# Optimization experiments

Measured on AMD Instinct MI355X. Metric: run time of the kernel, lower is better.

Reference implementation:

```python
import jax, jax.numpy as jnp
import numpy as np

MARGIN = 0.3

def _pairwise_euclid(x):
    # torch.cdist(x, x, p=2): [N, N] Euclidean distances, zero-safe sqrt
    sq_norms = jnp.sum(x * x, axis=1)                       # [N]
    sq = sq_norms[:, None] + sq_norms[None, :] - 2.0 * (x @ x.T)
    sq = jnp.maximum(sq, 0.0)
    safe = jnp.where(sq > 0.0, sq, 1.0)
    return jnp.where(sq > 0.0, jnp.sqrt(safe), 0.0)

def setup_inputs() -> dict:
    key = jax.random.key(0)
    k1, k2 = jax.random.split(key)
    features = jax.random.normal(k1, (4096, 512), dtype=jnp.float32)
    labels = jax.random.randint(k2, (4096,), 0, 256, dtype=jnp.int64)
    return {"features": features, "labels": labels}

def reference(features, labels):
    n = features.shape[0]
    dist = _pairwise_euclid(features)                       # [N, N]
    pos_mask = labels[:, None] == labels[None, :]           # includes self
    neg_inf = jnp.float32(-np.inf)
    pos_inf = jnp.float32(np.inf)
    hardest_pos = jnp.max(jnp.where(pos_mask, dist, neg_inf), axis=1)   # [N]
    hardest_neg = jnp.min(jnp.where(pos_mask, pos_inf, dist), axis=1)   # [N]
    valid = jnp.sum(pos_mask, axis=1) > 1                   # >1 positives incl. self
    per_row = jax.nn.relu(hardest_pos - hardest_neg + MARGIN)
    loss = jnp.sum(jnp.where(valid, per_row, 0.0)) / n
    return loss
```

## Files before the change

### kernel.cpp

```cpp
#include <hip/hip_runtime.h>

#define NROWS 4096
#define DIM   512
#define MARGIN 0.3f

typedef _Float16 f16;
typedef _Float16 f16x8 __attribute__((ext_vector_type(8)));
typedef float    f32x4 __attribute__((ext_vector_type(4)));

__global__ void prep_kernel(const float* __restrict__ X,
                            float* __restrict__ norms, f16* __restrict__ Xh,
                            unsigned* __restrict__ hp, unsigned* __restrict__ hn) {
    int t = threadIdx.x;
    int wave = t >> 6, lane = t & 63;
    int row  = blockIdx.x * 4 + wave;
    const float4* p = (const float4*)(X + (size_t)row * DIM + lane * 8);
    float4 a = p[0], b = p[1];
    float s = a.x*a.x + a.y*a.y + a.z*a.z + a.w*a.w
            + b.x*b.x + b.y*b.y + b.z*b.z + b.w*b.w;
    #pragma unroll
    for (int o = 32; o; o >>= 1) s += __shfl_xor(s, o);
    if (lane == 0) norms[row] = s;

    f16x8 h;
    h[0] = (f16)a.x; h[1] = (f16)a.y; h[2] = (f16)a.z; h[3] = (f16)a.w;
    h[4] = (f16)b.x; h[5] = (f16)b.y; h[6] = (f16)b.z; h[7] = (f16)b.w;
    int K0 = lane >> 2, c = lane & 3;
    int R = row >> 7, rw = row & 127, rg = rw >> 4, r = rw & 15;
    size_t unit = (size_t)(R * 16 + K0) * 512 + rg * 64 + c * 16 + r;
    *(f16x8*)(Xh + unit * 8) = h;

    int g = blockIdx.x * 256 + t;
    if (g < NROWS) { hp[g] = 0u; hn[g] = 0x7f800000u; }
}

__device__ inline void gload_lds16(const f16* g, f16* l) {
    __builtin_amdgcn_global_load_lds(
        (const __attribute__((address_space(1))) void*)g,
        (__attribute__((address_space(3))) void*)l, 16, 0, 0);
}

__device__ inline void stage_tile(const f16* __restrict__ At, const f16* __restrict__ Bt,
                                  f16* buf, int qb, int lane) {
    const f16* base = (qb < 512) ? (At + (size_t)qb * 8) : (Bt + (size_t)(qb - 512) * 8);
    #pragma unroll
    for (int c2 = 0; c2 < 4; ++c2)
        gload_lds16(base + (size_t)(c2 * 64 + lane) * 8, buf + (size_t)(qb + c2 * 64) * 8);
}

__global__ __launch_bounds__(256, 3) void mfma_dist_kernel(
        const f16* __restrict__ Xh, const int* __restrict__ labels,
        const float* __restrict__ norms,
        unsigned* __restrict__ hp, unsigned* __restrict__ hn) {
    __shared__ __align__(16) f16 S[3 * 8192];

    const int t    = threadIdx.x;
    const int lane = t & 63, w = t >> 6;
    const int l15  = lane & 15, l4 = lane >> 4;

    int bthw = blockIdx.x;
    int bt = (bthw & 7) * 66 + (bthw >> 3);

    int bx = (int)((sqrtf(8.0f * bt + 1.0f) - 1.0f) * 0.5f);
    while ((bx + 1) * (bx + 2) / 2 <= bt) ++bx;
    while (bx * (bx + 1) / 2 > bt) --bx;
    int by = bt - bx * (bx + 1) / 2;

    const int wr = w >> 1, wc = w & 1;
    const int qb = w * 256;

    const f16* Abase = Xh + (size_t)(by * 16) * 4096;
    const f16* Bbase = Xh + (size_t)(bx * 16) * 4096;

    f32x4 zero = {0.f, 0.f, 0.f, 0.f};
    f32x4 acc[4][4];
    #pragma unroll
    for (int m = 0; m < 4; ++m)
        #pragma unroll
        for (int n = 0; n < 4; ++n) acc[m][n] = zero;

    stage_tile(Abase,        Bbase,        S,        qb, lane);
    stage_tile(Abase + 4096, Bbase + 4096, S + 8192, qb, lane);
    __builtin_amdgcn_sched_barrier(0);

    #pragma unroll
    for (int kt = 0; kt < 16; ++kt) {
        f16* cur = S + (kt % 3) * 8192;
        if (kt == 15) asm volatile("s_waitcnt vmcnt(0)" ::: "memory");
        else          asm volatile("s_waitcnt vmcnt(4)" ::: "memory");
        __builtin_amdgcn_sched_barrier(0);
        __builtin_amdgcn_s_barrier();
        __builtin_amdgcn_sched_barrier(0);

        if (kt + 2 < 16)
            stage_tile(Abase + (size_t)(kt + 2) * 4096,
                       Bbase + (size_t)(kt + 2) * 4096,
                       S + ((kt + 2) % 3) * 8192, qb, lane);
        __builtin_amdgcn_sched_barrier(0);

        f16x8 af[4], bf[4];
        #pragma unroll
        for (int m = 0; m < 4; ++m)
            af[m] = *(const f16x8*)&cur[(size_t)((wr * 4 + m) * 64 + l4 * 16 + l15) * 8];
        #pragma unroll
        for (int n = 0; n < 4; ++n)
            bf[n] = *(const f16x8*)&cur[(size_t)(512 + (wc * 4 + n) * 64 + l4 * 16 + l15) * 8];
        #pragma unroll
        for (int m = 0; m < 4; ++m)
            #pragma unroll
            for (int n = 0; n < 4; ++n)
                acc[m][n] = __builtin_amdgcn_mfma_f32_16x16x32_f16(af[m], bf[n], acc[m][n], 0, 0, 0);
        __builtin_amdgcn_sched_barrier(0);
    }

    const int wrow = by * 128 + wr * 64;
    const int wcol = bx * 128 + wc * 64;
    const float FINF = __uint_as_float(0x7f800000u);

    int lj[4]; float nj[4];
    #pragma unroll
    for (int n = 0; n < 4; ++n) {
        int gc = wcol + n * 16 + l15; lj[n] = labels[gc]; nj[n] = norms[gc];
    }
    int li[16]; float ni[16];
    #pragma unroll
    for (int m = 0; m < 4; ++m)
        #pragma unroll
        for (int r = 0; r < 4; ++r) {
            int gr = wrow + m * 16 + l4 * 4 + r;
            li[m * 4 + r] = labels[gr]; ni[m * 4 + r] = norms[gr];
        }

    float cp[4], cn[4];
    #pragma unroll
    for (int n = 0; n < 4; ++n) { cp[n] = 0.f; cn[n] = FINF; }

    #pragma unroll
    for (int m = 0; m < 4; ++m) {
        #pragma unroll
        for (int r = 0; r < 4; ++r) {
            float rp = 0.f, rn = FINF;
            #pragma unroll
            for (int n = 0; n < 4; ++n) {
                float sq = fmaxf(fmaf(-2.f, acc[m][n][r], ni[m * 4 + r] + nj[n]), 0.f);
                bool same = (li[m * 4 + r] == lj[n]);
                rp = same ? fmaxf(rp, sq) : rp;
                rn = same ? rn : fminf(rn, sq);
                cp[n] = same ? fmaxf(cp[n], sq) : cp[n];
                cn[n] = same ? cn[n] : fminf(cn[n], sq);
            }
            #pragma unroll
            for (int o = 8; o; o >>= 1) {
                rp = fmaxf(rp, __shfl_xor(rp, o));
                rn = fminf(rn, __shfl_xor(rn, o));
            }
            if (l15 == 0) {
                int gr = wrow + m * 16 + l4 * 4 + r;
                atomicMax(&hp[gr], __float_as_uint(rp));
                atomicMin(&hn[gr], __float_as_uint(rn));
            }
        }
    }
    #pragma unroll
    for (int n = 0; n < 4; ++n) {
        float p = cp[n], q = cn[n];
        p = fmaxf(p, __shfl_xor(p, 16)); q = fminf(q, __shfl_xor(q, 16));
        p = fmaxf(p, __shfl_xor(p, 32)); q = fminf(q, __shfl_xor(q, 32));
        if (l4 == 0) {
            int gc = wcol + n * 16 + l15;
            atomicMax(&hp[gc], __float_as_uint(p));
            atomicMin(&hn[gc], __float_as_uint(q));
        }
    }
}

__global__ void norms_init_kernel(const float* __restrict__ X,
                                  float* __restrict__ norms,
                                  unsigned* __restrict__ hp, unsigned* __restrict__ hn) {
    int wave = threadIdx.x >> 6;
    int lane = threadIdx.x & 63;
    int row  = blockIdx.x * 4 + wave;
    const float4* xr = (const float4*)(X + (size_t)row * DIM);
    float4 a = xr[lane];
    float4 b = xr[lane + 64];
    float s = a.x*a.x + a.y*a.y + a.z*a.z + a.w*a.w
            + b.x*b.x + b.y*b.y + b.z*b.z + b.w*b.w;
    #pragma unroll
    for (int o = 32; o; o >>= 1) s += __shfl_xor(s, o);
    if (lane == 0) norms[row] = s;
    int g = blockIdx.x * 256 + threadIdx.x;
    if (g < NROWS) { hp[g] = 0u; hn[g] = 0x7f800000u; }
}

#define BK  32
#define PAD 68
__global__ __launch_bounds__(256) void dist_fp32_kernel(
        const float* __restrict__ X, const int* __restrict__ labels,
        const float* __restrict__ norms,
        unsigned* __restrict__ hp, unsigned* __restrict__ hn) {
    __shared__ __align__(16) float As[BK][PAD];
    __shared__ __align__(16) float Bs[BK][PAD];
    const int t  = threadIdx.x;
    const int tx = t & 15, ty = t >> 4;
    const int row0 = blockIdx.y * 64, col0 = blockIdx.x * 64;

    float acc[4][4] = {};
    for (int k0 = 0; k0 < DIM; k0 += BK) {
        #pragma unroll
        for (int l = 0; l < 2; ++l) {
            int idx = t + l * 256;
            int r = idx >> 3, fc = idx & 7;
            float4 va = *(const float4*)(X + (size_t)(row0 + r) * DIM + k0 + fc * 4);
            float4 vb = *(const float4*)(X + (size_t)(col0 + r) * DIM + k0 + fc * 4);
            As[fc*4+0][r] = va.x; As[fc*4+1][r] = va.y;
            As[fc*4+2][r] = va.z; As[fc*4+3][r] = va.w;
            Bs[fc*4+0][r] = vb.x; Bs[fc*4+1][r] = vb.y;
            Bs[fc*4+2][r] = vb.z; Bs[fc*4+3][r] = vb.w;
        }
        __syncthreads();
        #pragma unroll
        for (int kk = 0; kk < BK; ++kk) {
            float4 a = *(const float4*)&As[kk][ty * 4];
            float4 b = *(const float4*)&Bs[kk][tx * 4];
            float av[4] = {a.x, a.y, a.z, a.w};
            float bv[4] = {b.x, b.y, b.z, b.w};
            #pragma unroll
            for (int m = 0; m < 4; ++m)
                #pragma unroll
                for (int n = 0; n < 4; ++n)
                    acc[m][n] = fmaf(av[m], bv[n], acc[m][n]);
        }
        __syncthreads();
    }
    int li[4], lj[4]; float ni[4], nj[4];
    #pragma unroll
    for (int m = 0; m < 4; ++m) {
        int gi = row0 + ty * 4 + m; li[m] = labels[gi]; ni[m] = norms[gi];
    }
    #pragma unroll
    for (int n = 0; n < 4; ++n) {
        int gj = col0 + tx * 4 + n; lj[n] = labels[gj]; nj[n] = norms[gj];
    }
    #pragma unroll
    for (int m = 0; m < 4; ++m) {
        float pmax = 0.0f;
        float nmin = __uint_as_float(0x7f800000u);
        #pragma unroll
        for (int n = 0; n < 4; ++n) {
            float sq = fmaxf(ni[m] + nj[n] - 2.0f * acc[m][n], 0.0f);
            if (li[m] == lj[n]) pmax = fmaxf(pmax, sq);
            else                nmin = fminf(nmin, sq);
        }
        #pragma unroll
        for (int o = 8; o; o >>= 1) {
            pmax = fmaxf(pmax, __shfl_xor(pmax, o));
            nmin = fminf(nmin, __shfl_xor(nmin, o));
        }
        if (tx == 0) {
            int gi = row0 + ty * 4 + m;
            atomicMax(&hp[gi], __float_as_uint(pmax));
            atomicMin(&hn[gi], __float_as_uint(nmin));
        }
    }
}

__global__ __launch_bounds__(1024) void finalize_kernel(
        const unsigned* __restrict__ hp, const unsigned* __restrict__ hn,
        const int* __restrict__ labels, float* __restrict__ out) {
    __shared__ int hist[256];
    __shared__ float wsum[16];
    int t = threadIdx.x;
    if (t < 256) hist[t] = 0;
    __syncthreads();
    int4 lab = ((const int4*)labels)[t];
    atomicAdd(&hist[lab.x], 1); atomicAdd(&hist[lab.y], 1);
    atomicAdd(&hist[lab.z], 1); atomicAdd(&hist[lab.w], 1);
    __syncthreads();
    uint4 hp4 = ((const uint4*)hp)[t];
    uint4 hn4 = ((const uint4*)hn)[t];
    int      lv[4]  = {lab.x, lab.y, lab.z, lab.w};
    unsigned hpv[4] = {hp4.x, hp4.y, hp4.z, hp4.w};
    unsigned hnv[4] = {hn4.x, hn4.y, hn4.z, hn4.w};
    float v = 0.f;
    #pragma unroll
    for (int j = 0; j < 4; ++j) {
        float hpd = sqrtf(__uint_as_float(hpv[j]));
        float hnd = sqrtf(__uint_as_float(hnv[j]));
        if (hist[lv[j]] > 1) v += fmaxf(hpd - hnd + MARGIN, 0.f);
    }
    #pragma unroll
    for (int o = 32; o; o >>= 1) v += __shfl_xor(v, o);
    int lane = t & 63, wv = t >> 6;
    if (lane == 0) wsum[wv] = v;
    __syncthreads();
    if (t == 0) {
        float s = 0.f;
        #pragma unroll
        for (int i = 0; i < 16; ++i) s += wsum[i];
        out[0] = s / (float)NROWS;
    }
}

extern "C" void kernel_launch(void* const* d_in, const int* in_sizes, int n_in,
                              void* d_out, int out_size, void* d_ws, size_t ws_size,
                              hipStream_t stream) {
    const float* X      = (const float*)d_in[0];
    const int*   labels = (const int*)d_in[1];
    float* ws = (float*)d_ws;
    float*    norms = ws;
    unsigned* hp    = (unsigned*)(ws + 4096);
    unsigned* hn    = (unsigned*)(ws + 8192);
    f16*      Xh    = (f16*)((char*)d_ws + 65536);
    float*    out   = (float*)d_out;

    const size_t need = 65536 + (size_t)NROWS * DIM * sizeof(f16);

    if (ws_size >= need) {
        hipLaunchKernelGGL(prep_kernel,      dim3(NROWS/4), dim3(256), 0, stream,
                           X, norms, Xh, hp, hn);
        hipLaunchKernelGGL(mfma_dist_kernel, dim3(528),     dim3(256), 0, stream,
                           Xh, labels, norms, hp, hn);
    } else {
        hipLaunchKernelGGL(norms_init_kernel, dim3(NROWS/4), dim3(256), 0, stream, X, norms, hp, hn);
        hipLaunchKernelGGL(dist_fp32_kernel,  dim3(64, 64),  dim3(256), 0, stream, X, labels, norms, hp, hn);
    }
    hipLaunchKernelGGL(finalize_kernel, dim3(1), dim3(1024), 0, stream, hp, hn, labels, out);
}
```

Measured before the change: 33.94 us.

## Split triangular tiles into 64x128 halves and raise occupancy

The distance tile shrinks from 128x128 to 64x128 rows by columns. A new triangular mapping enumerates half-row-block tiles, doubling the grid to 1056 blocks, and the LDS ring buffer and per-wave accumulators are reduced to match. Launch bounds rise to 4 blocks per CU, and MFMA sections are wrapped in s_setprio to favour math waves. The aim is better load balance and latency hiding across the 256 CUs, paid for with more redundant B-tile loads from global memory and more atomic reductions in the epilogue.

```diff
diff --git a/kernel.cpp b/kernel.cpp
--- a/kernel.cpp
+++ b/kernel.cpp
@@ -40,80 +40,87 @@
         (__attribute__((address_space(3))) void*)l, 16, 0, 0);
 }
 
-__device__ inline void stage_tile(const f16* __restrict__ At, const f16* __restrict__ Bt,
+__device__ inline void stage_half(const f16* __restrict__ Ab, const f16* __restrict__ Bb,
                                   f16* buf, int qb, int lane) {
-    const f16* base = (qb < 512) ? (At + (size_t)qb * 8) : (Bt + (size_t)(qb - 512) * 8);
-    #pragma unroll
-    for (int c2 = 0; c2 < 4; ++c2)
-        gload_lds16(base + (size_t)(c2 * 64 + lane) * 8, buf + (size_t)(qb + c2 * 64) * 8);
-}
-
-__global__ __launch_bounds__(256, 3) void mfma_dist_kernel(
+    #pragma unroll
+    for (int c2 = 0; c2 < 3; ++c2) {
+        int q = qb + c2 * 64 + lane;
+        const f16* src = (q < 256) ? (Ab + (size_t)q * 8) : (Bb + (size_t)(q - 256) * 8);
+        gload_lds16(src, buf + (size_t)(qb + c2 * 64) * 8);
+    }
+}
+
+__global__ __launch_bounds__(256, 4) void mfma_dist_kernel(
         const f16* __restrict__ Xh, const int* __restrict__ labels,
         const float* __restrict__ norms,
         unsigned* __restrict__ hp, unsigned* __restrict__ hn) {
-    __shared__ __align__(16) f16 S[3 * 8192];
+    __shared__ __align__(16) f16 S[3 * 6144];
 
     const int t    = threadIdx.x;
     const int lane = t & 63, w = t >> 6;
     const int l15  = lane & 15, l4 = lane >> 4;
 
     int bthw = blockIdx.x;
-    int bt = (bthw & 7) * 66 + (bthw >> 3);
-
-    int bx = (int)((sqrtf(8.0f * bt + 1.0f) - 1.0f) * 0.5f);
-    while ((bx + 1) * (bx + 2) / 2 <= bt) ++bx;
-    while (bx * (bx + 1) / 2 > bt) --bx;
-    int by = bt - bx * (bx + 1) / 2;
+    int bt = (bthw & 7) * 132 + (bthw >> 3);
+
+    int s = (int)sqrtf((float)bt);
+    while ((s + 1) * (s + 1) <= bt) ++s;
+    while (s * s > bt) --s;
+    int by2, bx;
+    if (bt < s * (s + 1)) { by2 = 2 * s - 1; bx = bt - s * s; }
+    else                  { by2 = 2 * s;     bx = bt - s * (s + 1); }
 
     const int wr = w >> 1, wc = w & 1;
-    const int qb = w * 256;
-
-    const f16* Abase = Xh + (size_t)(by * 16) * 4096;
-    const f16* Bbase = Xh + (size_t)(bx * 16) * 4096;
+    const int qb = w * 192;
+
+    const int R = by2 >> 1, half = by2 & 1;
+    const f16* Ab = Xh + (size_t)(R * 16) * 4096 + half * 2048;
+    const f16* Bb = Xh + (size_t)(bx * 16) * 4096;
 
     f32x4 zero = {0.f, 0.f, 0.f, 0.f};
-    f32x4 acc[4][4];
-    #pragma unroll
-    for (int m = 0; m < 4; ++m)
+    f32x4 acc[2][4];
+    #pragma unroll
+    for (int m = 0; m < 2; ++m)
         #pragma unroll
         for (int n = 0; n < 4; ++n) acc[m][n] = zero;
 
-    stage_tile(Abase,        Bbase,        S,        qb, lane);
-    stage_tile(Abase + 4096, Bbase + 4096, S + 8192, qb, lane);
+    stage_half(Ab,        Bb,        S,        qb, lane);
+    stage_half(Ab + 4096, Bb + 4096, S + 6144, qb, lane);
     __builtin_amdgcn_sched_barrier(0);
 
     #pragma unroll
     for (int kt = 0; kt < 16; ++kt) {
-        f16* cur = S + (kt % 3) * 8192;
+        f16* cur = S + (kt % 3) * 6144;
         if (kt == 15) asm volatile("s_waitcnt vmcnt(0)" ::: "memory");
-        else          asm volatile("s_waitcnt vmcnt(4)" ::: "memory");
+        else          asm volatile("s_waitcnt vmcnt(3)" ::: "memory");
         __builtin_amdgcn_sched_barrier(0);
         __builtin_amdgcn_s_barrier();
         __builtin_amdgcn_sched_barrier(0);
 
         if (kt + 2 < 16)
-            stage_tile(Abase + (size_t)(kt + 2) * 4096,
-                       Bbase + (size_t)(kt + 2) * 4096,
-                       S + ((kt + 2) % 3) * 8192, qb, lane);
+            stage_half(Ab + (size_t)(kt + 2) * 4096,
+                       Bb + (size_t)(kt + 2) * 4096,
+                       S + ((kt + 2) % 3) * 6144, qb, lane);
         __builtin_amdgcn_sched_barrier(0);
 
-        f16x8 af[4], bf[4];
-        #pragma unroll
-        for (int m = 0; m < 4; ++m)
-            af[m] = *(const f16x8*)&cur[(size_t)((wr * 4 + m) * 64 + l4 * 16 + l15) * 8];
+        f16x8 af[2], bf[4];
+        #pragma unroll
+        for (int m = 0; m < 2; ++m)
+            af[m] = *(const f16x8*)&cur[(size_t)((wr * 2 + m) * 64 + l4 * 16 + l15) * 8];
         #pragma unroll
         for (int n = 0; n < 4; ++n)
-            bf[n] = *(const f16x8*)&cur[(size_t)(512 + (wc * 4 + n) * 64 + l4 * 16 + l15) * 8];
-        #pragma unroll
-        for (int m = 0; m < 4; ++m)
+            bf[n] = *(const f16x8*)&cur[(size_t)(256 + (wc * 4 + n) * 64 + l4 * 16 + l15) * 8];
+        __builtin_amdgcn_s_setprio(1);
+        #pragma unroll
+        for (int m = 0; m < 2; ++m)
             #pragma unroll
             for (int n = 0; n < 4; ++n)
                 acc[m][n] = __builtin_amdgcn_mfma_f32_16x16x32_f16(af[m], bf[n], acc[m][n], 0, 0, 0);
+        __builtin_amdgcn_s_setprio(0);
         __builtin_amdgcn_sched_barrier(0);
     }
 
-    const int wrow = by * 128 + wr * 64;
+    const int wrow = by2 * 64 + wr * 32;
     const int wcol = bx * 128 + wc * 64;
     const float FINF = __uint_as_float(0x7f800000u);
 
@@ -122,9 +129,9 @@
     for (int n = 0; n < 4; ++n) {
         int gc = wcol + n * 16 + l15; lj[n] = labels[gc]; nj[n] = norms[gc];
     }
-    int li[16]; float ni[16];
-    #pragma unroll
-    for (int m = 0; m < 4; ++m)
+    int li[8]; float ni[8];
+    #pragma unroll
+    for (int m = 0; m < 2; ++m)
         #pragma unroll
         for (int r = 0; r < 4; ++r) {
             int gr = wrow + m * 16 + l4 * 4 + r;
@@ -136,7 +143,7 @@
     for (int n = 0; n < 4; ++n) { cp[n] = 0.f; cn[n] = FINF; }
 
     #pragma unroll
-    for (int m = 0; m < 4; ++m) {
+    for (int m = 0; m < 2; ++m) {
         #pragma unroll
         for (int r = 0; r < 4; ++r) {
             float rp = 0.f, rn = FINF;
@@ -318,7 +325,7 @@
     if (ws_size >= need) {
         hipLaunchKernelGGL(prep_kernel,      dim3(NROWS/4), dim3(256), 0, stream,
                            X, norms, Xh, hp, hn);
-        hipLaunchKernelGGL(mfma_dist_kernel, dim3(528),     dim3(256), 0, stream,
+        hipLaunchKernelGGL(mfma_dist_kernel, dim3(1056),    dim3(256), 0, stream,
                            Xh, labels, norms, hp, hn);
     } else {
         hipLaunchKernelGGL(norms_init_kernel, dim3(NROWS/4), dim3(256), 0, stream, X, norms, hp, hn);
```

After: 38.76 us. +14.2%, slower.
